# Optimization experiments

Hardware: AMD Instinct MI355X
Metric: run time of the kernel (lower is better)

The kernel has to match this reference:

```python
import jax, jax.numpy as jnp
import numpy as np

NUM_GRAPHS = 128
N_NODES = 50000
N_EDGES = 400000
EMB = 384
L = 5
BN_EPS = 1e-5


def _bn(h, gamma, beta):
    # training-mode BatchNorm1d over the node/edge dim (biased variance, like torch)
    m = h.mean(axis=0)
    v = h.var(axis=0)
    return gamma * (h - m) * jax.lax.rsqrt(v + BN_EPS) + beta


def setup_inputs() -> dict:
    key = jax.random.key(0)
    ks = jax.random.split(key, 16)
    batch = jnp.sort(jax.random.randint(ks[0], (N_NODES,), 0, NUM_GRAPHS))
    x = jax.random.randint(ks[1], (N_NODES, 9), 0, 64)
    edge_index = jax.random.randint(ks[2], (2, N_EDGES), 0, N_NODES)
    edge_attr = jax.random.randint(ks[3], (N_EDGES, 3), 0, 8)
    s = 0.05
    atom_emb = jax.random.normal(ks[4], (9, 64, EMB), jnp.float32) * s
    bond_emb = jax.random.normal(ks[5], (3, 8, EMB), jnp.float32) * s
    # per-layer GINE MLP params, stacked over layers
    W1 = jax.random.normal(ks[6], (L, EMB, 2 * EMB), jnp.float32) * (1.0 / np.sqrt(EMB))
    b1 = jnp.zeros((L, 2 * EMB), jnp.float32)
    g1 = jnp.ones((L, 2 * EMB), jnp.float32)
    be1 = jnp.zeros((L, 2 * EMB), jnp.float32)
    W2 = jax.random.normal(ks[7], (L, 2 * EMB, EMB), jnp.float32) * (1.0 / np.sqrt(2 * EMB))
    b2 = jnp.zeros((L, EMB), jnp.float32)
    # outer per-layer BatchNorm params
    gbn = jnp.ones((L, EMB), jnp.float32)
    bbn = jnp.zeros((L, EMB), jnp.float32)
    return {"batch": batch, "x": x, "edge_index": edge_index, "edge_attr": edge_attr,
            "atom_emb": atom_emb, "bond_emb": bond_emb,
            "W1": W1, "b1": b1, "g1": g1, "be1": be1,
            "W2": W2, "b2": b2, "gbn": gbn, "bbn": bbn}


def reference(batch, x, edge_index, edge_attr, atom_emb, bond_emb,
              W1, b1, g1, be1, W2, b2, gbn, bbn):
    # AtomEncoder / BondEncoder: sum of per-column embedding lookups
    h = atom_emb[jnp.arange(9), x].sum(axis=1)          # [N, EMB]
    e = bond_emb[jnp.arange(3), edge_attr].sum(axis=1)  # [E, EMB]
    src, dst = edge_index[0], edge_index[1]
    for i in range(W1.shape[0]):
        # GINEConv: sum_j relu(x_j + e_ij)  (edge_weight defaults to ones)
        msg = jax.nn.relu(h[src] + e)                                   # [E, EMB]
        agg = jax.ops.segment_sum(msg, dst, num_segments=N_NODES)      # [N, EMB]
        z = h + agg                                                     # (1+eps)*x_i + agg, eps=0
        # MLP: Linear -> BN -> ReLU -> Linear
        z = z @ W1[i] + b1[i]
        z = jax.nn.relu(_bn(z, g1[i], be1[i]))
        z = z @ W2[i] + b2[i]
        # outer BN + ReLU (drop_ratio = 0.0)
        h = jax.nn.relu(_bn(z, gbn[i], bbn[i]))
    # standard pooling: global_add_pool
    graph_emb = jax.ops.segment_sum(h, batch, num_segments=NUM_GRAPHS)  # [G, EMB]
    return graph_emb, h
```

## Files before the change

### kernel.cpp

```cpp
#include <hip/hip_runtime.h>
#include <stdint.h>

#define NN 50000
#define NE 400000
#define EMB 384
#define NH 768
#define NL 5

typedef __bf16 bf16x8_t __attribute__((ext_vector_type(8)));
typedef float  f32x4_t  __attribute__((ext_vector_type(4)));

__device__ __forceinline__ float bflo(uint32_t u){ union{uint32_t u;float f;} v; v.u = u<<16; return v.f; }
__device__ __forceinline__ float bfhi(uint32_t u){ union{uint32_t u;float f;} v; v.u = u & 0xffff0000u; return v.f; }
__device__ __forceinline__ uint16_t f2bf(float f){
  union{float f;uint32_t u;} v; v.f=f;
  uint32_t r = v.u + 0x7fffu + ((v.u>>16)&1u);
  return (uint16_t)(r>>16);
}
__device__ __forceinline__ uint32_t bfpack2(float a, float b){
  return (uint32_t)f2bf(a) | ((uint32_t)f2bf(b)<<16);
}
__device__ __forceinline__ uint32_t bfpack2h(float a, float b){
  uint32_t r;
  asm("v_cvt_pk_bf16_f32 %0, %1, %2" : "=v"(r) : "v"(a), "v"(b));
  return r;
}
__device__ __forceinline__ bf16x8_t as_bf16x8(uint4 u){
  union{uint4 a; bf16x8_t b;} c; c.a = u; return c.b;
}

__device__ __forceinline__ void gld16(uint16_t* ldsp, const uint16_t* gp){
  __builtin_amdgcn_global_load_lds(
      (const __attribute__((address_space(1))) uint32_t*)gp,
      (__attribute__((address_space(3))) uint32_t*)ldsp,
      16, 0, 0);
}

__global__ void hist_kernel(const int* __restrict__ dst, int* __restrict__ count){
  int i = blockIdx.x*256 + threadIdx.x;
  if (i < NE) atomicAdd(&count[dst[i]], 1);
}
__global__ void scan_block_sum(const int* __restrict__ count, int* __restrict__ bsum, int n){
  __shared__ int s[256];
  int i = blockIdx.x*256 + threadIdx.x;
  s[threadIdx.x] = (i<n) ? count[i] : 0;
  __syncthreads();
  for (int st=128; st>0; st>>=1){
    if (threadIdx.x < st) s[threadIdx.x] += s[threadIdx.x+st];
    __syncthreads();
  }
  if (threadIdx.x==0) bsum[blockIdx.x] = s[0];
}
__global__ void scan_excl_small(int* __restrict__ bsum, int nb){
  __shared__ int s[256];
  int t = threadIdx.x;
  int v = (t<nb) ? bsum[t] : 0;
  s[t] = v;
  __syncthreads();
  for (int st=1; st<256; st<<=1){
    int u = (t>=st) ? s[t-st] : 0;
    __syncthreads();
    s[t] += u;
    __syncthreads();
  }
  if (t<nb) bsum[t] = s[t] - v;
}
__global__ void scan_final(const int* __restrict__ count, const int* __restrict__ bsum,
                           int* __restrict__ rowptr, int* __restrict__ cursor, int n){
  __shared__ int s[256];
  int t = threadIdx.x;
  int i = blockIdx.x*256 + t;
  int v = (i<n) ? count[i] : 0;
  s[t] = v;
  __syncthreads();
  for (int st=1; st<256; st<<=1){
    int u = (t>=st) ? s[t-st] : 0;
    __syncthreads();
    s[t] += u;
    __syncthreads();
  }
  int off = bsum[blockIdx.x] + s[t] - v;
  if (i < n){
    rowptr[i] = off; cursor[i] = off;
    if (i == n-1) rowptr[n] = off + v;
  }
}
__global__ void scatter_kernel(const int* __restrict__ dst, const int* __restrict__ src,
                               const int* __restrict__ eattr, int* __restrict__ cursor,
                               int* __restrict__ csr_src, int* __restrict__ csr_code){
  int e = blockIdx.x*256 + threadIdx.x;
  if (e < NE){
    int p = atomicAdd(&cursor[dst[e]], 1);
    csr_src[p] = src[e];
    csr_code[p] = eattr[e*3] | (eattr[e*3+1]<<3) | (eattr[e*3+2]<<6);
  }
}

__global__ void build_bond(const float* __restrict__ bemb, uint16_t* __restrict__ bt){
  const int code = blockIdx.x;
  const int t0 = code&7, t1=(code>>3)&7, t2=code>>6;
  const int c = threadIdx.x;
  const float2 a = ((const float2*)(bemb + (size_t)( 0+t0)*EMB))[c];
  const float2 b = ((const float2*)(bemb + (size_t)( 8+t1)*EMB))[c];
  const float2 d = ((const float2*)(bemb + (size_t)(16+t2)*EMB))[c];
  ((uint32_t*)(bt + (size_t)code*EMB))[c] = bfpack2(a.x+b.x+d.x, a.y+b.y+d.y);
}

__global__ void transpose_w(const float* __restrict__ in, uint16_t* __restrict__ outp,
                            int R, int Cc){
  __shared__ float tile[32][33];
  const size_t lo = (size_t)blockIdx.z * R * Cc;
  int cb = blockIdx.x*32, rb = blockIdx.y*32;
  int r = rb + threadIdx.y, c = cb + threadIdx.x;
  if (r < R && c < Cc) tile[threadIdx.y][threadIdx.x] = in[lo + (size_t)r*Cc + c];
  __syncthreads();
  int orr = cb + threadIdx.y, occ = rb + threadIdx.x;
  if (orr < Cc && occ < R) outp[lo + (size_t)orr*R + occ] = f2bf(tile[threadIdx.x][threadIdx.y]);
}

__global__ __launch_bounds__(256) void atom_encode(
    const int* __restrict__ x, const float* __restrict__ aemb,
    uint16_t* __restrict__ h){
  const int w = threadIdx.x >> 6, lane = threadIdx.x & 63;
  const int i = blockIdx.x*4 + w;
  if (i >= NN) return;
  float a0=0,a1=0,a2=0,a3=0,a4=0,a5=0;
  #pragma unroll
  for (int k=0;k<9;k++){
    const int idx = x[i*9+k];
    const float2* p = (const float2*)(aemb + ((size_t)(k*64+idx))*EMB) + lane*3;
    float2 u0=p[0], u1=p[1], u2=p[2];
    a0+=u0.x; a1+=u0.y; a2+=u1.x; a3+=u1.y; a4+=u2.x; a5+=u2.y;
  }
  uint32_t* hp = (uint32_t*)(h + (size_t)i*EMB) + lane*3;
  hp[0]=bfpack2(a0,a1); hp[1]=bfpack2(a2,a3); hp[2]=bfpack2(a4,a5);
}

template<int BNREL>
__global__ __launch_bounds__(256) void agg_kernel(
    const uint16_t* __restrict__ in, const uint16_t* __restrict__ bondt,
    const float* __restrict__ scale, const float* __restrict__ shift,
    const int* __restrict__ rowptr, const int* __restrict__ csr_src,
    const int* __restrict__ csr_code, uint16_t* __restrict__ za){
  const int w = threadIdx.x >> 6, lane = threadIdx.x & 63;
  const int i = blockIdx.x*4 + w;
  if (i >= NN) return;

  float sc0=0,sc1=0,sc2=0,sc3=0,sc4=0,sc5=0, sh0=0,sh1=0,sh2=0,sh3=0,sh4=0,sh5=0;
  if (BNREL){
    const int c = lane*6;
    sc0=scale[c]; sc1=scale[c+1]; sc2=scale[c+2]; sc3=scale[c+3]; sc4=scale[c+4]; sc5=scale[c+5];
    sh0=shift[c]; sh1=shift[c+1]; sh2=shift[c+2]; sh3=shift[c+3]; sh4=shift[c+4]; sh5=shift[c+5];
  }

  const uint32_t* hs = (const uint32_t*)(in + (size_t)i*EMB) + lane*3;
  uint32_t s0=hs[0], s1=hs[1], s2=hs[2];
  float a0,a1,a2,a3,a4,a5;
  if (BNREL){
    a0 = fmaxf(bflo(s0)*sc0+sh0, 0.f); a1 = fmaxf(bfhi(s0)*sc1+sh1, 0.f);
    a2 = fmaxf(bflo(s1)*sc2+sh2, 0.f); a3 = fmaxf(bfhi(s1)*sc3+sh3, 0.f);
    a4 = fmaxf(bflo(s2)*sc4+sh4, 0.f); a5 = fmaxf(bfhi(s2)*sc5+sh5, 0.f);
  } else {
    a0 = bflo(s0); a1 = bfhi(s0); a2 = bflo(s1); a3 = bfhi(s1); a4 = bflo(s2); a5 = bfhi(s2);
  }

  const int rs = rowptr[i], re = rowptr[i+1];
  int k = rs;
  for (; k + 4 <= re; k += 4){
    int sj[4], cj[4];
    #pragma unroll
    for (int j=0;j<4;j++){ sj[j]=csr_src[k+j]; cj[j]=csr_code[k+j]; }
    uint32_t u[4][3], b[4][3];
    #pragma unroll
    for (int j=0;j<4;j++){
      const uint32_t* hp = (const uint32_t*)(in + (size_t)sj[j]*EMB) + lane*3;
      u[j][0]=hp[0]; u[j][1]=hp[1]; u[j][2]=hp[2];
      const uint32_t* bp = (const uint32_t*)(bondt + (size_t)cj[j]*EMB) + lane*3;
      b[j][0]=bp[0]; b[j][1]=bp[1]; b[j][2]=bp[2];
    }
    #pragma unroll
    for (int j=0;j<4;j++){
      float v0,v1,v2,v3,v4,v5;
      if (BNREL){
        v0 = fmaxf(bflo(u[j][0])*sc0+sh0, 0.f); v1 = fmaxf(bfhi(u[j][0])*sc1+sh1, 0.f);
        v2 = fmaxf(bflo(u[j][1])*sc2+sh2, 0.f); v3 = fmaxf(bfhi(u[j][1])*sc3+sh3, 0.f);
        v4 = fmaxf(bflo(u[j][2])*sc4+sh4, 0.f); v5 = fmaxf(bfhi(u[j][2])*sc5+sh5, 0.f);
      } else {
        v0=bflo(u[j][0]); v1=bfhi(u[j][0]); v2=bflo(u[j][1]);
        v3=bfhi(u[j][1]); v4=bflo(u[j][2]); v5=bfhi(u[j][2]);
      }
      a0 += fmaxf(v0+bflo(b[j][0]), 0.f); a1 += fmaxf(v1+bfhi(b[j][0]), 0.f);
      a2 += fmaxf(v2+bflo(b[j][1]), 0.f); a3 += fmaxf(v3+bfhi(b[j][1]), 0.f);
      a4 += fmaxf(v4+bflo(b[j][2]), 0.f); a5 += fmaxf(v5+bfhi(b[j][2]), 0.f);
    }
  }
  for (; k < re; k++){
    const int s = csr_src[k];
    const int code = csr_code[k];
    const uint32_t* hp = (const uint32_t*)(in + (size_t)s*EMB) + lane*3;
    uint32_t u0=hp[0], u1=hp[1], u2=hp[2];
    const uint32_t* bp = (const uint32_t*)(bondt + (size_t)code*EMB) + lane*3;
    uint32_t b0=bp[0], b1=bp[1], b2=bp[2];
    float v0,v1,v2,v3,v4,v5;
    if (BNREL){
      v0 = fmaxf(bflo(u0)*sc0+sh0, 0.f); v1 = fmaxf(bfhi(u0)*sc1+sh1, 0.f);
      v2 = fmaxf(bflo(u1)*sc2+sh2, 0.f); v3 = fmaxf(bfhi(u1)*sc3+sh3, 0.f);
      v4 = fmaxf(bflo(u2)*sc4+sh4, 0.f); v5 = fmaxf(bfhi(u2)*sc5+sh5, 0.f);
    } else {
      v0=bflo(u0); v1=bfhi(u0); v2=bflo(u1); v3=bfhi(u1); v4=bflo(u2); v5=bfhi(u2);
    }
    a0 += fmaxf(v0+bflo(b0), 0.f); a1 += fmaxf(v1+bfhi(b0), 0.f);
    a2 += fmaxf(v2+bflo(b1), 0.f); a3 += fmaxf(v3+bfhi(b1), 0.f);
    a4 += fmaxf(v4+bflo(b2), 0.f); a5 += fmaxf(v5+bfhi(b2), 0.f);
  }

  uint32_t* zp = (uint32_t*)(za + (size_t)i*EMB) + lane*3;
  zp[0] = bfpack2(a0,a1);
  zp[1] = bfpack2(a2,a3);
  zp[2] = bfpack2(a4,a5);
}

template<int BNA, int KK>
__global__ __launch_bounds__(256, BNA ? 2 : 3) void gemm_bt(
    const uint16_t* __restrict__ A, const uint16_t* __restrict__ Bt,
    const float* __restrict__ bias, const float* __restrict__ scA,
    const float* __restrict__ shA, uint16_t* __restrict__ C,
    float* __restrict__ stats, int M, int N, int nbr){
  constexpr int NPART = KK / 192;
  __shared__ __align__(16) uint16_t panel[6*4096];
  __shared__ float sAs[BNA ? KK : 1];
  __shared__ float hAs[BNA ? KK : 1];
  __shared__ float csum[128];
  __shared__ float csq[128];

  const int tid = threadIdx.x;
  const int nbc = N >> 7;
  const int xcd = blockIdx.x & 7;
  const int slot = blockIdx.x >> 3;
  const int bcol = slot % nbc;
  const int brow = (slot / nbc)*8 + xcd;
  if (brow >= nbr) return;
  const int rowbase = brow << 7;

  const int lane = tid & 63;
  const int w = tid >> 6;
  const int quad = lane >> 4, l16 = lane & 15;

  const int s0 = tid, s1 = 256 + tid;
  const int r0 = s0 & 127, r1 = s1 & 127;
  const int pb0 = bcol*128 + (r0 & 64) + ((r0 & 15) << 2) + ((r0 >> 4) & 3);
  const int pb1 = bcol*128 + (r1 & 64) + ((r1 & 15) << 2) + ((r1 >> 4) & 3);
  const uint16_t* gB0 = Bt + (size_t)pb0*KK + (s0>>7)*8;
  const uint16_t* gB1 = Bt + (size_t)pb1*KK + (s1>>7)*8;

  int rowA0 = rowbase + w*32 + l16;      if (rowA0 >= M) rowA0 = M-1;
  int rowA1 = rowbase + w*32 + 16 + l16; if (rowA1 >= M) rowA1 = M-1;
  const uint16_t* gA0 = A + (size_t)rowA0*KK + quad*8;
  const uint16_t* gA1 = A + (size_t)rowA1*KK + quad*8;

  if (BNA){
    for (int i = tid; i < KK; i += 256){ sAs[i] = scA[i]; hAs[i] = shA[i]; }
  }

  f32x4_t acc[2][2][4];
  #pragma unroll
  for (int mi=0;mi<2;mi++)
    #pragma unroll
    for (int g=0;g<2;g++)
      #pragma unroll
      for (int nj=0;nj<4;nj++)
        acc[mi][g][nj] = (f32x4_t){0.f,0.f,0.f,0.f};

  for (int part = 0; part < NPART; ++part){
    const int k0 = part*192;
    if (part) __syncthreads();
    #pragma unroll
    for (int sl = 0; sl < 6; ++sl){
      gld16(&panel[sl*4096 + s0*8], gB0 + k0 + sl*32);
      gld16(&panel[sl*4096 + s1*8], gB1 + k0 + sl*32);
    }
    uint4 ca0 = *(const uint4*)(gA0 + k0);
    uint4 ca1 = *(const uint4*)(gA1 + k0);
    __syncthreads();

    uint4 na0, na1;
    #pragma unroll
    for (int kq = 0; kq < 6; ++kq){
      if (kq < 5){
        na0 = *(const uint4*)(gA0 + k0 + (kq+1)*32);
        na1 = *(const uint4*)(gA1 + k0 + (kq+1)*32);
      }
      bf16x8_t fa0, fa1;
      if (BNA){
        const int kb = k0 + kq*32 + quad*8;
        float4 sv0 = *(const float4*)&sAs[kb];
        float4 sv1 = *(const float4*)&sAs[kb+4];
        float4 hv0 = *(const float4*)&hAs[kb];
        float4 hv1 = *(const float4*)&hAs[kb+4];
        float e0,e1,e2,e3,e4,e5,e6,e7;
        e0=fmaxf(bflo(ca0.x)*sv0.x+hv0.x,0.f); e1=fmaxf(bfhi(ca0.x)*sv0.y+hv0.y,0.f);
        e2=fmaxf(bflo(ca0.y)*sv0.z+hv0.z,0.f); e3=fmaxf(bfhi(ca0.y)*sv0.w+hv0.w,0.f);
        e4=fmaxf(bflo(ca0.z)*sv1.x+hv1.x,0.f); e5=fmaxf(bfhi(ca0.z)*sv1.y+hv1.y,0.f);
        e6=fmaxf(bflo(ca0.w)*sv1.z+hv1.z,0.f); e7=fmaxf(bfhi(ca0.w)*sv1.w+hv1.w,0.f);
        fa0 = as_bf16x8(make_uint4(bfpack2h(e0,e1),bfpack2h(e2,e3),bfpack2h(e4,e5),bfpack2h(e6,e7)));
        e0=fmaxf(bflo(ca1.x)*sv0.x+hv0.x,0.f); e1=fmaxf(bfhi(ca1.x)*sv0.y+hv0.y,0.f);
        e2=fmaxf(bflo(ca1.y)*sv0.z+hv0.z,0.f); e3=fmaxf(bfhi(ca1.y)*sv0.w+hv0.w,0.f);
        e4=fmaxf(bflo(ca1.z)*sv1.x+hv1.x,0.f); e5=fmaxf(bfhi(ca1.z)*sv1.y+hv1.y,0.f);
        e6=fmaxf(bflo(ca1.w)*sv1.z+hv1.z,0.f); e7=fmaxf(bfhi(ca1.w)*sv1.w+hv1.w,0.f);
        fa1 = as_bf16x8(make_uint4(bfpack2h(e0,e1),bfpack2h(e2,e3),bfpack2h(e4,e5),bfpack2h(e6,e7)));
      } else {
        fa0 = as_bf16x8(ca0);
        fa1 = as_bf16x8(ca1);
      }
      #pragma unroll
      for (int g=0; g<2; ++g)
        #pragma unroll
        for (int nj=0; nj<4; ++nj){
          bf16x8_t fb = *(const bf16x8_t*)&panel[kq*4096 + (quad*128 + g*64 + nj*16 + l16)*8];
          acc[0][g][nj] = __builtin_amdgcn_mfma_f32_16x16x32_bf16(fa0, fb, acc[0][g][nj], 0,0,0);
          acc[1][g][nj] = __builtin_amdgcn_mfma_f32_16x16x32_bf16(fa1, fb, acc[1][g][nj], 0,0,0);
        }
      ca0 = na0; ca1 = na1;
    }
  }

  if (tid < 128){ csum[tid]=0.f; csq[tid]=0.f; }
  __syncthreads();

  const int colbase = bcol*128 + l16*4;
  float bv[2][4], ssum[2][4], sq[2][4];
  #pragma unroll
  for (int g=0;g<2;g++)
    #pragma unroll
    for (int nj=0;nj<4;nj++){
      bv[g][nj] = bias[colbase + g*64 + nj];
      ssum[g][nj] = 0.f; sq[g][nj] = 0.f;
    }

  #pragma unroll
  for (int mi=0;mi<2;mi++){
    #pragma unroll
    for (int r=0;r<4;r++){
      const int grow = rowbase + w*32 + mi*16 + quad*4 + r;
      if (grow < M){
        #pragma unroll
        for (int g=0;g<2;g++){
          float v0 = acc[mi][g][0][r] + bv[g][0];
          float v1 = acc[mi][g][1][r] + bv[g][1];
          float v2 = acc[mi][g][2][r] + bv[g][2];
          float v3 = acc[mi][g][3][r] + bv[g][3];
          uint2 pk = make_uint2(bfpack2h(v0,v1), bfpack2h(v2,v3));
          *(uint2*)(C + (size_t)grow*N + colbase + g*64) = pk;
          ssum[g][0]+=v0; ssum[g][1]+=v1; ssum[g][2]+=v2; ssum[g][3]+=v3;
          sq[g][0]+=v0*v0; sq[g][1]+=v1*v1; sq[g][2]+=v2*v2; sq[g][3]+=v3*v3;
        }
      }
    }
  }
  #pragma unroll
  for (int g=0;g<2;g++)
    #pragma unroll
    for (int nj=0;nj<4;nj++){
      ssum[g][nj] += __shfl_xor(ssum[g][nj], 16); ssum[g][nj] += __shfl_xor(ssum[g][nj], 32);
      sq[g][nj]   += __shfl_xor(sq[g][nj],   16); sq[g][nj]   += __shfl_xor(sq[g][nj],   32);
    }
  if (quad == 0){
    #pragma unroll
    for (int g=0;g<2;g++)
      #pragma unroll
      for (int nj=0;nj<4;nj++){
        atomicAdd(&csum[g*64 + l16*4 + nj], ssum[g][nj]);
        atomicAdd(&csq [g*64 + l16*4 + nj], sq[g][nj]);
      }
  }
  __syncthreads();
  if (tid < 128){
    atomicAdd(&stats[bcol*128 + tid], csum[tid]);
    atomicAdd(&stats[N + bcol*128 + tid], csq[tid]);
  }
}

__global__ void bn_finalize(float* __restrict__ stats, const float* __restrict__ gamma,
                            const float* __restrict__ beta, float* __restrict__ scale,
                            float* __restrict__ shift, int n, float invM){
  int c = blockIdx.x*256 + threadIdx.x;
  if (c < n){
    float mean = stats[c]*invM;
    float var  = stats[n+c]*invM - mean*mean;
    float sc = gamma[c] * rsqrtf(var + 1e-5f);
    scale[c] = sc;
    shift[c] = beta[c] - mean*sc;
    stats[c] = 0.f;
    stats[n+c] = 0.f;
  }
}

__global__ void bn_relu_final(const uint16_t* __restrict__ u, const float* __restrict__ scale,
                              const float* __restrict__ shift, float* __restrict__ hf){
  int i = blockIdx.x*256 + threadIdx.x;
  const int total2 = NN*EMB/2;
  if (i >= total2) return;
  uint32_t v = ((const uint32_t*)u)[i];
  int c = (i*2) % EMB;
  float f0 = fmaxf(bflo(v)*scale[c  ] + shift[c  ], 0.f);
  float f1 = fmaxf(bfhi(v)*scale[c+1] + shift[c+1], 0.f);
  ((float2*)hf)[i] = make_float2(f0, f1);
}

__global__ void pool_kernel(const float* __restrict__ h, const int* __restrict__ batch,
                            float* __restrict__ pool){
  __shared__ int bs[64];
  int c = threadIdx.x;
  int n0 = blockIdx.x*64;
  if (c < 64){ int i = n0 + c; bs[c] = (i < NN) ? batch[i] : -1; }
  __syncthreads();
  float sum = 0.f; int cur = -1;
  for (int tt=0; tt<64; tt++){
    int i = n0 + tt;
    if (i >= NN) break;
    int g = bs[tt];
    float v = h[(size_t)i*EMB + c];
    if (g != cur){
      if (cur >= 0) atomicAdd(&pool[(size_t)cur*EMB + c], sum);
      cur = g; sum = v;
    } else sum += v;
  }
  if (cur >= 0) atomicAdd(&pool[(size_t)cur*EMB + c], sum);
}
__global__ void pool_to_out(const float* __restrict__ pool, float* __restrict__ outp){
  int i = blockIdx.x*256 + threadIdx.x;
  if (i < 128*EMB) outp[i] = pool[i];
}

extern "C" void kernel_launch(void* const* d_in, const int* in_sizes, int n_in,
                              void* d_out, int out_size, void* d_ws, size_t ws_size,
                              hipStream_t stream){
  (void)in_sizes; (void)n_in; (void)out_size; (void)ws_size;
  const int* batch = (const int*)d_in[0];
  const int* x     = (const int*)d_in[1];
  const int* eidx  = (const int*)d_in[2];
  const int* eattr = (const int*)d_in[3];
  const float* aemb = (const float*)d_in[4];
  const float* bemb = (const float*)d_in[5];
  const float* W1 = (const float*)d_in[6];
  const float* b1 = (const float*)d_in[7];
  const float* g1 = (const float*)d_in[8];
  const float* be1= (const float*)d_in[9];
  const float* W2 = (const float*)d_in[10];
  const float* b2 = (const float*)d_in[11];
  const float* gbn= (const float*)d_in[12];
  const float* bbn= (const float*)d_in[13];
  float* out = (float*)d_out;

  char* base = (char*)d_ws;
  size_t off = 0;
  auto alloc = [&](size_t bytes) -> void* {
    void* p = base + off;
    off = (off + bytes + 255) & ~(size_t)255;
    return p;
  };
  uint16_t* za   = (uint16_t*)alloc((size_t)NN*EMB*2);
  uint16_t* zm   = (uint16_t*)alloc((size_t)NN*EMB*2);
  uint16_t* t    = (uint16_t*)alloc((size_t)NN*NH*2);
  uint16_t* W1t  = (uint16_t*)alloc((size_t)NL*NH*EMB*2);
  uint16_t* W2t  = (uint16_t*)alloc((size_t)NL*EMB*NH*2);
  uint16_t* bondt= (uint16_t*)alloc((size_t)512*EMB*2);
  float* stats1  = (float*)alloc(NH*2*4);
  float* stats2  = (float*)alloc(EMB*2*4);
  float* scale1  = (float*)alloc(NH*4);
  float* shift1  = (float*)alloc(NH*4);
  float* scale2  = (float*)alloc(EMB*4);
  float* shift2  = (float*)alloc(EMB*4);
  float* pool    = (float*)alloc(128*EMB*4);
  int* count   = (int*)alloc((size_t)NN*4);
  int* rowptr  = (int*)alloc((size_t)(NN+1)*4);
  int* cursor  = (int*)alloc((size_t)NN*4);
  int* bsum    = (int*)alloc(256*4);
  int* csr_src = (int*)alloc((size_t)NE*4);
  int* csr_code= (int*)alloc((size_t)NE*4);

  const int* esrc = eidx;
  const int* edst = eidx + NE;
  const int nsb = (NN + 255)/256;

  hipMemsetAsync(count, 0, (size_t)NN*4, stream);
  hist_kernel<<<(NE+255)/256, 256, 0, stream>>>(edst, count);
  scan_block_sum<<<nsb, 256, 0, stream>>>(count, bsum, NN);
  scan_excl_small<<<1, 256, 0, stream>>>(bsum, nsb);
  scan_final<<<nsb, 256, 0, stream>>>(count, bsum, rowptr, cursor, NN);
  scatter_kernel<<<(NE+255)/256, 256, 0, stream>>>(edst, esrc, eattr, cursor, csr_src, csr_code);

  build_bond<<<512, 192, 0, stream>>>(bemb, bondt);
  transpose_w<<<dim3(NH/32, EMB/32, NL), dim3(32,32), 0, stream>>>(W1, W1t, EMB, NH);
  transpose_w<<<dim3(EMB/32, NH/32, NL), dim3(32,32), 0, stream>>>(W2, W2t, NH, EMB);

  atom_encode<<<NN/4, 256, 0, stream>>>(x, aemb, zm);
  hipMemsetAsync(pool, 0, (size_t)128*EMB*4, stream);
  hipMemsetAsync(stats1, 0, (size_t)(6144 + 3072), stream);

  const int nbr = (NN + 127)/128;
  const int nbrr = ((nbr + 7)/8)*8;
  const int g1blocks = nbrr*(NH/128);
  const int g2blocks = nbrr*(EMB/128);
  for (int l = 0; l < NL; l++){
    if (l == 0)
      agg_kernel<0><<<NN/4, 256, 0, stream>>>(zm, bondt, nullptr, nullptr,
                                              rowptr, csr_src, csr_code, za);
    else
      agg_kernel<1><<<NN/4, 256, 0, stream>>>(zm, bondt, scale2, shift2,
                                              rowptr, csr_src, csr_code, za);
    gemm_bt<0, EMB><<<g1blocks, 256, 0, stream>>>(
        za, W1t + (size_t)l*NH*EMB, b1 + l*NH, nullptr, nullptr, t, stats1, NN, NH, nbr);
    bn_finalize<<<(NH+255)/256, 256, 0, stream>>>(stats1, g1 + l*NH, be1 + l*NH,
                                                  scale1, shift1, NH, 1.0f/NN);
    gemm_bt<1, NH><<<g2blocks, 256, 0, stream>>>(
        t, W2t + (size_t)l*EMB*NH, b2 + l*EMB, scale1, shift1, zm, stats2, NN, EMB, nbr);
    bn_finalize<<<(EMB+255)/256, 256, 0, stream>>>(stats2, gbn + l*EMB, bbn + l*EMB,
                                                   scale2, shift2, EMB, 1.0f/NN);
  }
  bn_relu_final<<<(NN*EMB/2 + 255)/256, 256, 0, stream>>>(zm, scale2, shift2, out + 128*EMB);
  pool_kernel<<<(NN+63)/64, 384, 0, stream>>>(out + 128*EMB, batch, pool);
  pool_to_out<<<(128*EMB+255)/256, 256, 0, stream>>>(pool, out);
}
```

Measured before the change: 1.354 ms.

## Double-buffer B panels in GEMM and raise occupancy target to 4 blocks

```diff
diff --git a/kernel.cpp b/kernel.cpp
--- a/kernel.cpp
+++ b/kernel.cpp
@@ -221,13 +221,14 @@
 }
 
 template<int BNA, int KK>
-__global__ __launch_bounds__(256, BNA ? 2 : 3) void gemm_bt(
+__global__ __launch_bounds__(256, 4) void gemm_bt(
     const uint16_t* __restrict__ A, const uint16_t* __restrict__ Bt,
     const float* __restrict__ bias, const float* __restrict__ scA,
     const float* __restrict__ shA, uint16_t* __restrict__ C,
     float* __restrict__ stats, int M, int N, int nbr){
-  constexpr int NPART = KK / 192;
-  __shared__ __align__(16) uint16_t panel[6*4096];
+  constexpr int NK = KK/32;
+  constexpr int NPART = NK/2;
+  __shared__ __align__(16) uint16_t panel[2][2][4096];
   __shared__ float sAs[BNA ? KK : 1];
   __shared__ float hAs[BNA ? KK : 1];
   __shared__ float csum[128];
@@ -271,28 +272,37 @@
       for (int nj=0;nj<4;nj++)
         acc[mi][g][nj] = (f32x4_t){0.f,0.f,0.f,0.f};
 
-  for (int part = 0; part < NPART; ++part){
-    const int k0 = part*192;
-    if (part) __syncthreads();
-    #pragma unroll
-    for (int sl = 0; sl < 6; ++sl){
-      gld16(&panel[sl*4096 + s0*8], gB0 + k0 + sl*32);
-      gld16(&panel[sl*4096 + s1*8], gB1 + k0 + sl*32);
-    }
-    uint4 ca0 = *(const uint4*)(gA0 + k0);
-    uint4 ca1 = *(const uint4*)(gA1 + k0);
-    __syncthreads();
-
-    uint4 na0, na1;
-    #pragma unroll
-    for (int kq = 0; kq < 6; ++kq){
-      if (kq < 5){
-        na0 = *(const uint4*)(gA0 + k0 + (kq+1)*32);
-        na1 = *(const uint4*)(gA1 + k0 + (kq+1)*32);
-      }
+  uint4 ar0[4], ar1[4];
+
+  gld16(&panel[0][0][s0*8], gB0);
+  gld16(&panel[0][0][s1*8], gB1);
+  gld16(&panel[0][1][s0*8], gB0 + 32);
+  gld16(&panel[0][1][s1*8], gB1 + 32);
+  ar0[0] = *(const uint4*)(gA0);      ar1[0] = *(const uint4*)(gA1);
+  ar0[1] = *(const uint4*)(gA0 + 32); ar1[1] = *(const uint4*)(gA1 + 32);
+  __syncthreads();
+
+  #pragma unroll
+  for (int p = 0; p < NPART; ++p){
+    if (p + 1 < NPART){
+      const int kf = (p+1)*2;
+      gld16(&panel[(p+1)&1][0][s0*8], gB0 + kf*32);
+      gld16(&panel[(p+1)&1][0][s1*8], gB1 + kf*32);
+      gld16(&panel[(p+1)&1][1][s0*8], gB0 + (kf+1)*32);
+      gld16(&panel[(p+1)&1][1][s1*8], gB1 + (kf+1)*32);
+      ar0[kf&3]     = *(const uint4*)(gA0 + kf*32);
+      ar1[kf&3]     = *(const uint4*)(gA1 + kf*32);
+      ar0[(kf+1)&3] = *(const uint4*)(gA0 + (kf+1)*32);
+      ar1[(kf+1)&3] = *(const uint4*)(gA1 + (kf+1)*32);
+    }
+    #pragma unroll
+    for (int s = 0; s < 2; ++s){
+      const int kq = p*2 + s;
+      const uint4 ca0 = ar0[kq&3];
+      const uint4 ca1 = ar1[kq&3];
       bf16x8_t fa0, fa1;
       if (BNA){
-        const int kb = k0 + kq*32 + quad*8;
+        const int kb = kq*32 + quad*8;
         float4 sv0 = *(const float4*)&sAs[kb];
         float4 sv1 = *(const float4*)&sAs[kb+4];
         float4 hv0 = *(const float4*)&hAs[kb];
@@ -316,12 +326,12 @@
       for (int g=0; g<2; ++g)
         #pragma unroll
         for (int nj=0; nj<4; ++nj){
-          bf16x8_t fb = *(const bf16x8_t*)&panel[kq*4096 + (quad*128 + g*64 + nj*16 + l16)*8];
+          bf16x8_t fb = *(const bf16x8_t*)&panel[p&1][s][(quad*128 + g*64 + nj*16 + l16)*8];
           acc[0][g][nj] = __builtin_amdgcn_mfma_f32_16x16x32_bf16(fa0, fb, acc[0][g][nj], 0,0,0);
           acc[1][g][nj] = __builtin_amdgcn_mfma_f32_16x16x32_bf16(fa1, fb, acc[1][g][nj], 0,0,0);
         }
-      ca0 = na0; ca1 = na1;
-    }
+    }
+    __syncthreads();
   }
 
   if (tid < 128){ csum[tid]=0.f; csq[tid]=0.f; }
```

Measured after the change: 1.306 ms. 1.04x faster.
